# Kernel tuning notes

Hardware: AMD Instinct MI355X
Metric: run time of the kernel (lower is better)

Reference implementation:

```python
import jax, jax.numpy as jnp
import numpy as np
import math

MAX2D = 1001        # max_2d_position_embeddings
COORD = 128         # coordinate_size
SHAPE = 128         # shape_size
PE = 384            # pos_embed_size
HID = 768           # layout_hidden_size
PAD = 0             # pad_token_id
EPS = 1e-12
INIT = 1024         # sinusoidal init_size
BIG = 100000000


def sinusoidal_table(num_embeddings=INIT, dim=PE, padding_idx=PAD):
    half = dim // 2
    freq = np.exp(np.arange(half, dtype=np.float32) * (-math.log(10000.0) / (half - 1)))
    ang = np.arange(num_embeddings, dtype=np.float32)[:, None] * freq[None, :]
    tab = np.concatenate([np.sin(ang), np.cos(ang)], axis=1)
    if padding_idx is not None:
        tab[padding_idx, :] = 0.0
    return jnp.asarray(tab, dtype=jnp.float32)


def setup_inputs() -> dict:
    key = jax.random.key(0)
    ks = jax.random.split(key, 16)
    B, L = 2, 1024
    x1 = jax.random.randint(ks[0], (B, L), 0, 501, dtype=jnp.int32)
    y1 = jax.random.randint(ks[1], (B, L), 0, 501, dtype=jnp.int32)
    w = jax.random.randint(ks[2], (B, L), 0, 500, dtype=jnp.int32)
    h = jax.random.randint(ks[3], (B, L), 0, 500, dtype=jnp.int32)
    bbox = jnp.stack([x1, y1, x1 + w, y1 + h], axis=-1)  # [B,L,4], 0..1000
    attention_mask = jnp.ones((B, L), dtype=jnp.int32)
    s = 0.02
    inp = {
        'bbox': bbox,
        'attention_mask': attention_mask,
        'x_tab': jax.random.normal(ks[4], (MAX2D, COORD), jnp.float32) * s,
        'y_tab': jax.random.normal(ks[5], (MAX2D, COORD), jnp.float32) * s,
        'h_tab': jax.random.normal(ks[6], (MAX2D, SHAPE), jnp.float32) * s,
        'w_tab': jax.random.normal(ks[7], (MAX2D, SHAPE), jnp.float32) * s,
        'W_tl_w': jax.random.normal(ks[8], (HID, 2 * PE), jnp.float32) * s,
        'W_tl_b': jnp.zeros((HID,), jnp.float32),
        'W_tr_w': jax.random.normal(ks[9], (HID, 2 * PE), jnp.float32) * s,
        'W_tr_b': jnp.zeros((HID,), jnp.float32),
        'W_bl_w': jax.random.normal(ks[10], (HID, 2 * PE), jnp.float32) * s,
        'W_bl_b': jnp.zeros((HID,), jnp.float32),
        'W_br_w': jax.random.normal(ks[11], (HID, 2 * PE), jnp.float32) * s,
        'W_br_b': jnp.zeros((HID,), jnp.float32),
        'ln_g': jnp.ones((HID,), jnp.float32),
        'ln_b': jnp.zeros((HID,), jnp.float32),
        'params': 50,
    }
    return inp


def _knn_graph(bbox, mask, topk):
    # mask out padded boxes with a huge coordinate (matches masked_fill)
    bm = jnp.where((mask == 0)[..., None], BIG, bbox).astype(jnp.float32)
    xc = (bm[:, :, 0] + bm[:, :, 2]) / 2.0
    yc = (bm[:, :, 1] + bm[:, :, 3]) / 2.0
    dist = (xc[:, :, None] - xc[:, None, :]) ** 2 + (yc[:, :, None] - yc[:, None, :]) ** 2
    _, topk_index = jax.lax.top_k(-dist, topk)  # smallest distances
    topk_index = topk_index.astype(jnp.int32)
    B, L, _ = topk_index.shape
    lm = jnp.zeros((B, L, L), jnp.int32)
    b_ix = jnp.arange(B)[:, None, None]
    l_ix = jnp.arange(L)[None, :, None]
    lm = lm.at[b_ix, l_ix, topk_index].set(1)
    return topk_index, lm


def _rel_pos_emb(bbox, topk_index, sin_tab):
    # diff[b,i,k] = coord[b,i] - coord[b,topk_index[b,i,k]]
    gather = jax.vmap(lambda v, idx: v[idx])  # per-batch gather

    def diffs(c):
        d = c[:, :, None] - gather(c, topk_index)
        d = jnp.clip(d, 1 - MAX2D, MAX2D - 1)
        # torch negative indexing into the table wraps: idx % INIT
        return sin_tab[jnp.mod(d, INIT)]  # [B,L,K,PE]

    ex1 = diffs(bbox[:, :, 0])
    ey1 = diffs(bbox[:, :, 1])
    ex2 = diffs(bbox[:, :, 2])
    ey2 = diffs(bbox[:, :, 3])
    return ex1, ey1, ex2, ey2


def _linear(x, w, b):
    return jnp.einsum('blki,oi->blko', x, w) + b


def reference(bbox, attention_mask, x_tab, y_tab, h_tab, w_tab,
              W_tl_w, W_tl_b, W_tr_w, W_tr_b, W_bl_w, W_bl_b, W_br_w, W_br_b,
              ln_g, ln_b, params):
    sin_tab = sinusoidal_table()
    # spatial position embeddings
    layout_emb = jnp.concatenate([
        x_tab[bbox[:, :, 0]], y_tab[bbox[:, :, 1]],
        x_tab[bbox[:, :, 2]], y_tab[bbox[:, :, 3]],
        h_tab[bbox[:, :, 3] - bbox[:, :, 1]],
        w_tab[bbox[:, :, 2] - bbox[:, :, 0]],
    ], axis=-1)  # [B,L,HID]

    topk = min(bbox.shape[1], int(params))
    topk_index, local_mask = _knn_graph(bbox, attention_mask, topk)

    ex1, ey1, ex2, ey2 = _rel_pos_emb(bbox, topk_index, sin_tab)
    p = (_linear(jnp.concatenate([ex1, ey1], -1), W_tl_w, W_tl_b)
         + _linear(jnp.concatenate([ex2, ey1], -1), W_tr_w, W_tr_b)
         + _linear(jnp.concatenate([ex1, ey2], -1), W_bl_w, W_bl_b)
         + _linear(jnp.concatenate([ex2, ey2], -1), W_br_w, W_br_b))

    mu = jnp.mean(layout_emb, axis=-1, keepdims=True)
    var = jnp.mean((layout_emb - mu) ** 2, axis=-1, keepdims=True)
    layout_emb = (layout_emb - mu) / jnp.sqrt(var + EPS) * ln_g + ln_b
    # dropout is identity in eval mode
    return layout_emb, p, topk_index, local_mask
```

## Files before the change

### kernel.cpp

```cpp
#include <hip/hip_runtime.h>
#include <math.h>

namespace {
constexpr int B_ = 2;
constexpr int L_ = 1024;
constexpr int K_ = 50;
constexpr int HID_ = 768;
constexpr int PE_ = 384;
constexpr int HALF_ = 192;
constexpr int TROWS_ = 1024;

typedef float f32x4 __attribute__((ext_vector_type(4)));

constexpr long long OUT0 = 0;
constexpr long long OUT1 = OUT0 + (long long)B_ * L_ * HID_;
constexpr long long OUT2 = OUT1 + (long long)B_ * L_ * K_ * HID_;
constexpr long long OUT3 = OUT2 + (long long)B_ * L_ * K_;

constexpr long long WS_SIN = 0;
constexpr long long WS_T   = WS_SIN + (long long)TROWS_ * PE_;
constexpr long long WS_TI  = WS_T + 4LL * TROWS_ * HID_;
}

__global__ __launch_bounds__(192) void k_sin_tab(float* __restrict__ tab) {
    const int r = blockIdx.x;
    const int j = threadIdx.x;
    const float c = -0.04822168780092243f;
    float fr = expf((float)j * c);
    float ang = (float)r * fr;
    float s, co;
    if (r == 0) { s = 0.f; co = 0.f; } else { s = sinf(ang); co = cosf(ang); }
    tab[r * PE_ + j] = s;
    tab[r * PE_ + HALF_ + j] = co;
}

__global__ __launch_bounds__(256) void k_build_T(
    const float* __restrict__ sinT,
    const float* __restrict__ Wtl, const float* __restrict__ Wtr,
    const float* __restrict__ Wbl, const float* __restrict__ Wbr,
    const float* __restrict__ btl, const float* __restrict__ btr,
    const float* __restrict__ bbl, const float* __restrict__ bbr,
    float* __restrict__ Tout)
{
    const int t = blockIdx.z;
    const float* Wa; const float* Wb; int coff;
    if (t == 0)      { Wa = Wtl; Wb = Wbl; coff = 0; }
    else if (t == 1) { Wa = Wtr; Wb = Wbr; coff = 0; }
    else if (t == 2) { Wa = Wtl; Wb = Wtr; coff = PE_; }
    else             { Wa = Wbl; Wb = Wbr; coff = PE_; }

    __shared__ float As[32][65];
    __shared__ float Bs[32][65];
    const int tid = threadIdx.x;
    const int r0 = blockIdx.x * 64;
    const int o0 = blockIdx.y * 64;
    const int ty = tid >> 4, tx = tid & 15;
    float acc[4][4] = {{0.f, 0.f, 0.f, 0.f}, {0.f, 0.f, 0.f, 0.f},
                       {0.f, 0.f, 0.f, 0.f}, {0.f, 0.f, 0.f, 0.f}};

    for (int k0 = 0; k0 < PE_; k0 += 32) {
        #pragma unroll
        for (int s = 0; s < 8; ++s) {
            int l = s * 256 + tid;
            int rr = l >> 5, jj = l & 31;
            As[jj][rr] = sinT[(r0 + rr) * PE_ + k0 + jj];
            Bs[jj][rr] = Wa[(o0 + rr) * (2 * PE_) + coff + k0 + jj]
                       + Wb[(o0 + rr) * (2 * PE_) + coff + k0 + jj];
        }
        __syncthreads();
        #pragma unroll
        for (int kk = 0; kk < 32; ++kk) {
            float a[4], b[4];
            #pragma unroll
            for (int m = 0; m < 4; ++m) a[m] = As[kk][ty * 4 + m];
            #pragma unroll
            for (int n = 0; n < 4; ++n) b[n] = Bs[kk][tx * 4 + n];
            #pragma unroll
            for (int m = 0; m < 4; ++m)
                #pragma unroll
                for (int n = 0; n < 4; ++n)
                    acc[m][n] = fmaf(a[m], b[n], acc[m][n]);
        }
        __syncthreads();
    }

    #pragma unroll
    for (int m = 0; m < 4; ++m) {
        int r = r0 + ty * 4 + m;
        #pragma unroll
        for (int n = 0; n < 4; ++n) {
            int o = o0 + tx * 4 + n;
            float v = acc[m][n];
            if (t == 0) v += btl[o] + btr[o] + bbl[o] + bbr[o];
            Tout[(long long)t * TROWS_ * HID_ + (long long)r * HID_ + o] = v;
        }
    }
}

__device__ __forceinline__ float block_sum_256(float x, float* red) {
    #pragma unroll
    for (int off = 32; off > 0; off >>= 1) x += __shfl_xor(x, off, 64);
    const int wave = threadIdx.x >> 6;
    if ((threadIdx.x & 63) == 0) red[wave] = x;
    __syncthreads();
    float t = red[0] + red[1] + red[2] + red[3];
    __syncthreads();
    return t;
}

__global__ __launch_bounds__(256) void k_layout_emb(
    const int4* __restrict__ bbox, const float* __restrict__ xt,
    const float* __restrict__ yt, const float* __restrict__ ht,
    const float* __restrict__ wt, const float* __restrict__ g,
    const float* __restrict__ bb, float* __restrict__ out)
{
    __shared__ float red[4];
    const int tok = blockIdx.x;
    const int4 q = bbox[tok];
    const int tid = threadIdx.x;
    float v[3];
    #pragma unroll
    for (int s = 0; s < 3; ++s) {
        int e = tid + s * 256;
        int off = e & 127;
        int seg = e >> 7;
        float val;
        if (seg == 0)      val = xt[q.x * 128 + off];
        else if (seg == 1) val = yt[q.y * 128 + off];
        else if (seg == 2) val = xt[q.z * 128 + off];
        else if (seg == 3) val = yt[q.w * 128 + off];
        else if (seg == 4) val = ht[(q.w - q.y) * 128 + off];
        else               val = wt[(q.z - q.x) * 128 + off];
        v[s] = val;
    }
    float mu = block_sum_256(v[0] + v[1] + v[2], red) * (1.0f / 768.0f);
    float sq = 0.f;
    #pragma unroll
    for (int s = 0; s < 3; ++s) { float d = v[s] - mu; sq = fmaf(d, d, sq); }
    float var = block_sum_256(sq, red) * (1.0f / 768.0f);
    float inv = 1.0f / sqrtf(var + 1e-12f);
    float* orow = out + (long long)tok * HID_;
    #pragma unroll
    for (int s = 0; s < 3; ++s) {
        int e = tid + s * 256;
        __builtin_nontemporal_store((v[s] - mu) * inv * g[e] + bb[e], orow + e);
    }
}

__global__ __launch_bounds__(256) void k_topk(
    const int4* __restrict__ bbox, const int* __restrict__ am,
    float* __restrict__ topk_f, int* __restrict__ topk_i,
    float* __restrict__ mask)
{
    __shared__ float xs[L_], ys[L_];
    __shared__ float mrow_s[L_];
    __shared__ unsigned long long wmin[4];
    const int bx = blockIdx.x;
    const int b = bx >> 10;
    const int i = bx & 1023;
    const int tid = threadIdx.x;
    for (int j = tid; j < L_; j += 256) {
        int4 q = bbox[b * L_ + j];
        float x1, y1, x2, y2;
        if (am[b * L_ + j] == 0) { x1 = y1 = x2 = y2 = 1e8f; }
        else { x1 = (float)q.x; y1 = (float)q.y; x2 = (float)q.z; y2 = (float)q.w; }
        xs[j] = (x1 + x2) * 0.5f;
        ys[j] = (y1 + y2) * 0.5f;
        mrow_s[j] = 0.f;
    }
    __syncthreads();
    const float xq = xs[i], yq = ys[i];
    unsigned long long key[4];
    #pragma unroll
    for (int s = 0; s < 4; ++s) {
        int j = tid + s * 256;
        float dx = xq - xs[j], dy = yq - ys[j];
        float d = dx * dx + dy * dy;
        key[s] = ((unsigned long long)__float_as_uint(d) << 32) | (unsigned int)j;
    }
    const int lane = tid & 63, wave = tid >> 6;
    const long long obase = (long long)(b * L_ + i) * K_;
    for (int r = 0; r < K_; ++r) {
        unsigned long long m = key[0] < key[1] ? key[0] : key[1];
        unsigned long long m2 = key[2] < key[3] ? key[2] : key[3];
        if (m2 < m) m = m2;
        #pragma unroll
        for (int off = 1; off < 64; off <<= 1) {
            unsigned long long o = __shfl_xor(m, off, 64);
            if (o < m) m = o;
        }
        if (lane == 0) wmin[wave] = m;
        __syncthreads();
        unsigned long long mm = wmin[0] < wmin[1] ? wmin[0] : wmin[1];
        unsigned long long mb = wmin[2] < wmin[3] ? wmin[2] : wmin[3];
        if (mb < mm) mm = mb;
        if (tid == 0) {
            int w = (int)(mm & 0xffffffffu);
            topk_f[obase + r] = (float)w;
            topk_i[obase + r] = w;
            mrow_s[w] = 1.0f;
        }
        #pragma unroll
        for (int s = 0; s < 4; ++s) if (key[s] == mm) key[s] = ~0ULL;
        __syncthreads();
    }
    f32x4* mrow = (f32x4*)(mask + (long long)(b * L_ + i) * L_);
    const f32x4* src = (const f32x4*)mrow_s;
    __builtin_nontemporal_store(src[tid], mrow + tid);
}

__device__ __forceinline__ int wrapc(int d) {
    d = d < -1000 ? -1000 : (d > 1000 ? 1000 : d);
    return (d + 1024) & 1023;
}

__global__ __launch_bounds__(256) void k_passemble(
    const int4* __restrict__ bbox, const int* __restrict__ topk_i,
    const f32x4* __restrict__ T, float* __restrict__ p)
{
    const int row = blockIdx.x * 4 + (threadIdx.x >> 6);
    const int lane = threadIdx.x & 63;
    const int b = row / (L_ * K_);
    const int rem = row - b * (L_ * K_);
    const int i = rem / K_;
    const int j = topk_i[row];
    const int4 bi = bbox[b * L_ + i];
    const int4 bj = bbox[b * L_ + j];
    const f32x4* T1 = T + (long long)wrapc(bi.x - bj.x) * 192;
    const f32x4* T2 = T + 196608 + (long long)wrapc(bi.z - bj.z) * 192;
    const f32x4* T3 = T + 2 * 196608 + (long long)wrapc(bi.y - bj.y) * 192;
    const f32x4* T4 = T + 3 * 196608 + (long long)wrapc(bi.w - bj.w) * 192;
    f32x4* prow = (f32x4*)p + (long long)row * 192;
    #pragma unroll
    for (int u = 0; u < 3; ++u) {
        int f = lane + u * 64;
        f32x4 o = T1[f] + T2[f] + T3[f] + T4[f];
        __builtin_nontemporal_store(o, prow + f);
    }
}

extern "C" void kernel_launch(void* const* d_in, const int* in_sizes, int n_in,
                              void* d_out, int out_size, void* d_ws, size_t ws_size,
                              hipStream_t stream)
{
    const int4* bbox = (const int4*)d_in[0];
    const int* am    = (const int*)d_in[1];
    const float* xt  = (const float*)d_in[2];
    const float* yt  = (const float*)d_in[3];
    const float* ht  = (const float*)d_in[4];
    const float* wt  = (const float*)d_in[5];
    const float* Wtl = (const float*)d_in[6];
    const float* btl = (const float*)d_in[7];
    const float* Wtr = (const float*)d_in[8];
    const float* btr = (const float*)d_in[9];
    const float* Wbl = (const float*)d_in[10];
    const float* bbl = (const float*)d_in[11];
    const float* Wbr = (const float*)d_in[12];
    const float* bbr = (const float*)d_in[13];
    const float* lng = (const float*)d_in[14];
    const float* lnb = (const float*)d_in[15];

    float* out = (float*)d_out;
    float* ws = (float*)d_ws;
    float* sinT = ws + WS_SIN;
    float* T = ws + WS_T;
    int* topk_i = (int*)(ws + WS_TI);

    k_sin_tab<<<dim3(TROWS_), dim3(HALF_), 0, stream>>>(sinT);
    k_build_T<<<dim3(16, 12, 4), dim3(256), 0, stream>>>(
        sinT, Wtl, Wtr, Wbl, Wbr, btl, btr, bbl, bbr, T);
    k_layout_emb<<<dim3(B_ * L_), dim3(256), 0, stream>>>(
        bbox, xt, yt, ht, wt, lng, lnb, out + OUT0);
    k_topk<<<dim3(B_ * L_), dim3(256), 0, stream>>>(
        bbox, am, out + OUT2, topk_i, out + OUT3);
    k_passemble<<<dim3(B_ * L_ * K_ / 4), dim3(256), 0, stream>>>(
        bbox, topk_i, (const f32x4*)T, out + OUT1);
}
```

Before: 522.2 us.

## Merge table GEMM, top-k and layernorm kernels into one launch

```diff
diff --git a/kernel.cpp b/kernel.cpp
--- a/kernel.cpp
+++ b/kernel.cpp
@@ -20,6 +20,10 @@
 constexpr long long WS_SIN = 0;
 constexpr long long WS_T   = WS_SIN + (long long)TROWS_ * PE_;
 constexpr long long WS_TI  = WS_T + 4LL * TROWS_ * HID_;
+
+constexpr int GEMM_BLOCKS = 16 * 12 * 4;
+constexpr int TOPK_BLOCKS = B_ * L_;
+constexpr int LN_BLOCKS   = B_ * L_;
 }
 
 __global__ __launch_bounds__(192) void k_sin_tab(float* __restrict__ tab) {
@@ -34,68 +38,12 @@
     tab[r * PE_ + HALF_ + j] = co;
 }
 
-__global__ __launch_bounds__(256) void k_build_T(
-    const float* __restrict__ sinT,
-    const float* __restrict__ Wtl, const float* __restrict__ Wtr,
-    const float* __restrict__ Wbl, const float* __restrict__ Wbr,
-    const float* __restrict__ btl, const float* __restrict__ btr,
-    const float* __restrict__ bbl, const float* __restrict__ bbr,
-    float* __restrict__ Tout)
-{
-    const int t = blockIdx.z;
-    const float* Wa; const float* Wb; int coff;
-    if (t == 0)      { Wa = Wtl; Wb = Wbl; coff = 0; }
-    else if (t == 1) { Wa = Wtr; Wb = Wbr; coff = 0; }
-    else if (t == 2) { Wa = Wtl; Wb = Wtr; coff = PE_; }
-    else             { Wa = Wbl; Wb = Wbr; coff = PE_; }
-
-    __shared__ float As[32][65];
-    __shared__ float Bs[32][65];
-    const int tid = threadIdx.x;
-    const int r0 = blockIdx.x * 64;
-    const int o0 = blockIdx.y * 64;
-    const int ty = tid >> 4, tx = tid & 15;
-    float acc[4][4] = {{0.f, 0.f, 0.f, 0.f}, {0.f, 0.f, 0.f, 0.f},
-                       {0.f, 0.f, 0.f, 0.f}, {0.f, 0.f, 0.f, 0.f}};
-
-    for (int k0 = 0; k0 < PE_; k0 += 32) {
-        #pragma unroll
-        for (int s = 0; s < 8; ++s) {
-            int l = s * 256 + tid;
-            int rr = l >> 5, jj = l & 31;
-            As[jj][rr] = sinT[(r0 + rr) * PE_ + k0 + jj];
-            Bs[jj][rr] = Wa[(o0 + rr) * (2 * PE_) + coff + k0 + jj]
-                       + Wb[(o0 + rr) * (2 * PE_) + coff + k0 + jj];
-        }
-        __syncthreads();
-        #pragma unroll
-        for (int kk = 0; kk < 32; ++kk) {
-            float a[4], b[4];
-            #pragma unroll
-            for (int m = 0; m < 4; ++m) a[m] = As[kk][ty * 4 + m];
-            #pragma unroll
-            for (int n = 0; n < 4; ++n) b[n] = Bs[kk][tx * 4 + n];
-            #pragma unroll
-            for (int m = 0; m < 4; ++m)
-                #pragma unroll
-                for (int n = 0; n < 4; ++n)
-                    acc[m][n] = fmaf(a[m], b[n], acc[m][n]);
-        }
-        __syncthreads();
-    }
-
-    #pragma unroll
-    for (int m = 0; m < 4; ++m) {
-        int r = r0 + ty * 4 + m;
-        #pragma unroll
-        for (int n = 0; n < 4; ++n) {
-            int o = o0 + tx * 4 + n;
-            float v = acc[m][n];
-            if (t == 0) v += btl[o] + btr[o] + bbl[o] + bbr[o];
-            Tout[(long long)t * TROWS_ * HID_ + (long long)r * HID_ + o] = v;
-        }
-    }
-}
+union SMem {
+    struct { float As[32][68]; float Bs[32][68]; } g;
+    struct { float xs[L_]; float ys[L_]; float mrow[L_];
+             unsigned long long wmin[4]; } t;
+    struct { float red[4]; } l;
+};
 
 __device__ __forceinline__ float block_sum_256(float x, float* red) {
     #pragma unroll
@@ -108,105 +56,172 @@
     return t;
 }
 
-__global__ __launch_bounds__(256) void k_layout_emb(
-    const int4* __restrict__ bbox, const float* __restrict__ xt,
-    const float* __restrict__ yt, const float* __restrict__ ht,
-    const float* __restrict__ wt, const float* __restrict__ g,
-    const float* __restrict__ bb, float* __restrict__ out)
+__global__ __launch_bounds__(256) void k_mega(
+    const float* __restrict__ sinT,
+    const float* __restrict__ Wtl, const float* __restrict__ Wtr,
+    const float* __restrict__ Wbl, const float* __restrict__ Wbr,
+    const float* __restrict__ btl, const float* __restrict__ btr,
+    const float* __restrict__ bbl, const float* __restrict__ bbr,
+    float* __restrict__ Tout,
+    const int4* __restrict__ bbox, const int* __restrict__ am,
+    float* __restrict__ topk_f, int* __restrict__ topk_i, float* __restrict__ mask,
+    const float* __restrict__ xt, const float* __restrict__ yt,
+    const float* __restrict__ ht, const float* __restrict__ wt,
+    const float* __restrict__ lng, const float* __restrict__ lnb,
+    float* __restrict__ lout)
 {
-    __shared__ float red[4];
-    const int tok = blockIdx.x;
-    const int4 q = bbox[tok];
+    __shared__ SMem sm;
+    const int bid = blockIdx.x;
     const int tid = threadIdx.x;
-    float v[3];
-    #pragma unroll
-    for (int s = 0; s < 3; ++s) {
-        int e = tid + s * 256;
-        int off = e & 127;
-        int seg = e >> 7;
-        float val;
-        if (seg == 0)      val = xt[q.x * 128 + off];
-        else if (seg == 1) val = yt[q.y * 128 + off];
-        else if (seg == 2) val = xt[q.z * 128 + off];
-        else if (seg == 3) val = yt[q.w * 128 + off];
-        else if (seg == 4) val = ht[(q.w - q.y) * 128 + off];
-        else               val = wt[(q.z - q.x) * 128 + off];
-        v[s] = val;
-    }
-    float mu = block_sum_256(v[0] + v[1] + v[2], red) * (1.0f / 768.0f);
-    float sq = 0.f;
-    #pragma unroll
-    for (int s = 0; s < 3; ++s) { float d = v[s] - mu; sq = fmaf(d, d, sq); }
-    float var = block_sum_256(sq, red) * (1.0f / 768.0f);
-    float inv = 1.0f / sqrtf(var + 1e-12f);
-    float* orow = out + (long long)tok * HID_;
-    #pragma unroll
-    for (int s = 0; s < 3; ++s) {
-        int e = tid + s * 256;
-        __builtin_nontemporal_store((v[s] - mu) * inv * g[e] + bb[e], orow + e);
-    }
-}
-
-__global__ __launch_bounds__(256) void k_topk(
-    const int4* __restrict__ bbox, const int* __restrict__ am,
-    float* __restrict__ topk_f, int* __restrict__ topk_i,
-    float* __restrict__ mask)
-{
-    __shared__ float xs[L_], ys[L_];
-    __shared__ float mrow_s[L_];
-    __shared__ unsigned long long wmin[4];
-    const int bx = blockIdx.x;
-    const int b = bx >> 10;
-    const int i = bx & 1023;
-    const int tid = threadIdx.x;
-    for (int j = tid; j < L_; j += 256) {
-        int4 q = bbox[b * L_ + j];
-        float x1, y1, x2, y2;
-        if (am[b * L_ + j] == 0) { x1 = y1 = x2 = y2 = 1e8f; }
-        else { x1 = (float)q.x; y1 = (float)q.y; x2 = (float)q.z; y2 = (float)q.w; }
-        xs[j] = (x1 + x2) * 0.5f;
-        ys[j] = (y1 + y2) * 0.5f;
-        mrow_s[j] = 0.f;
-    }
-    __syncthreads();
-    const float xq = xs[i], yq = ys[i];
-    unsigned long long key[4];
-    #pragma unroll
-    for (int s = 0; s < 4; ++s) {
-        int j = tid + s * 256;
-        float dx = xq - xs[j], dy = yq - ys[j];
-        float d = dx * dx + dy * dy;
-        key[s] = ((unsigned long long)__float_as_uint(d) << 32) | (unsigned int)j;
-    }
-    const int lane = tid & 63, wave = tid >> 6;
-    const long long obase = (long long)(b * L_ + i) * K_;
-    for (int r = 0; r < K_; ++r) {
-        unsigned long long m = key[0] < key[1] ? key[0] : key[1];
-        unsigned long long m2 = key[2] < key[3] ? key[2] : key[3];
-        if (m2 < m) m = m2;
-        #pragma unroll
-        for (int off = 1; off < 64; off <<= 1) {
-            unsigned long long o = __shfl_xor(m, off, 64);
-            if (o < m) m = o;
-        }
-        if (lane == 0) wmin[wave] = m;
+
+    if (bid < GEMM_BLOCKS) {
+        const int t   = bid / 192;
+        const int rem = bid - t * 192;
+        const int rx  = rem & 15;
+        const int oy  = rem >> 4;
+        const float* Wa; const float* Wb; int coff;
+        if (t == 0)      { Wa = Wtl; Wb = Wbl; coff = 0; }
+        else if (t == 1) { Wa = Wtr; Wb = Wbr; coff = 0; }
+        else if (t == 2) { Wa = Wtl; Wb = Wtr; coff = PE_; }
+        else             { Wa = Wbl; Wb = Wbr; coff = PE_; }
+
+        const int r0 = rx * 64;
+        const int o0 = oy * 64;
+        const int ty = tid >> 4, tx = tid & 15;
+        float acc[4][4] = {{0.f,0.f,0.f,0.f},{0.f,0.f,0.f,0.f},
+                           {0.f,0.f,0.f,0.f},{0.f,0.f,0.f,0.f}};
+
+        for (int k0 = 0; k0 < PE_; k0 += 32) {
+            #pragma unroll
+            for (int s = 0; s < 2; ++s) {
+                int idx = s * 256 + tid;
+                int rr = idx >> 3, q = idx & 7;
+                f32x4 av = *(const f32x4*)&sinT[(r0 + rr) * PE_ + k0 + q * 4];
+                f32x4 w1 = *(const f32x4*)&Wa[(o0 + rr) * (2 * PE_) + coff + k0 + q * 4];
+                f32x4 w2 = *(const f32x4*)&Wb[(o0 + rr) * (2 * PE_) + coff + k0 + q * 4];
+                f32x4 bv = w1 + w2;
+                #pragma unroll
+                for (int c = 0; c < 4; ++c) {
+                    sm.g.As[q * 4 + c][rr] = av[c];
+                    sm.g.Bs[q * 4 + c][rr] = bv[c];
+                }
+            }
+            __syncthreads();
+            #pragma unroll
+            for (int kk = 0; kk < 32; ++kk) {
+                f32x4 a = *(const f32x4*)&sm.g.As[kk][ty * 4];
+                f32x4 b = *(const f32x4*)&sm.g.Bs[kk][tx * 4];
+                #pragma unroll
+                for (int m = 0; m < 4; ++m)
+                    #pragma unroll
+                    for (int n = 0; n < 4; ++n)
+                        acc[m][n] = fmaf(a[m], b[n], acc[m][n]);
+            }
+            __syncthreads();
+        }
+
+        #pragma unroll
+        for (int m = 0; m < 4; ++m) {
+            int r = r0 + ty * 4 + m;
+            f32x4 v;
+            #pragma unroll
+            for (int n = 0; n < 4; ++n) {
+                int o = o0 + tx * 4 + n;
+                float x = acc[m][n];
+                if (t == 0) x += btl[o] + btr[o] + bbl[o] + bbr[o];
+                v[n] = x;
+            }
+            *(f32x4*)&Tout[(long long)t * TROWS_ * HID_ + (long long)r * HID_ + o0 + tx * 4] = v;
+        }
+        return;
+    }
+
+    if (bid < GEMM_BLOCKS + TOPK_BLOCKS) {
+        const int bi = bid - GEMM_BLOCKS;
+        const int b = bi >> 10;
+        const int i = bi & 1023;
+        for (int j = tid; j < L_; j += 256) {
+            int4 q = bbox[b * L_ + j];
+            float x1, y1, x2, y2;
+            if (am[b * L_ + j] == 0) { x1 = y1 = x2 = y2 = 1e8f; }
+            else { x1 = (float)q.x; y1 = (float)q.y; x2 = (float)q.z; y2 = (float)q.w; }
+            sm.t.xs[j] = (x1 + x2) * 0.5f;
+            sm.t.ys[j] = (y1 + y2) * 0.5f;
+            sm.t.mrow[j] = 0.f;
+        }
         __syncthreads();
-        unsigned long long mm = wmin[0] < wmin[1] ? wmin[0] : wmin[1];
-        unsigned long long mb = wmin[2] < wmin[3] ? wmin[2] : wmin[3];
-        if (mb < mm) mm = mb;
-        if (tid == 0) {
-            int w = (int)(mm & 0xffffffffu);
-            topk_f[obase + r] = (float)w;
-            topk_i[obase + r] = w;
-            mrow_s[w] = 1.0f;
-        }
-        #pragma unroll
-        for (int s = 0; s < 4; ++s) if (key[s] == mm) key[s] = ~0ULL;
-        __syncthreads();
-    }
-    f32x4* mrow = (f32x4*)(mask + (long long)(b * L_ + i) * L_);
-    const f32x4* src = (const f32x4*)mrow_s;
-    __builtin_nontemporal_store(src[tid], mrow + tid);
+        const float xq = sm.t.xs[i], yq = sm.t.ys[i];
+        unsigned long long key[4];
+        #pragma unroll
+        for (int s = 0; s < 4; ++s) {
+            int j = tid + s * 256;
+            float dx = xq - sm.t.xs[j], dy = yq - sm.t.ys[j];
+            float d = dx * dx + dy * dy;
+            key[s] = ((unsigned long long)__float_as_uint(d) << 32) | (unsigned int)j;
+        }
+        const int lane = tid & 63, wave = tid >> 6;
+        const long long obase = (long long)(b * L_ + i) * K_;
+        for (int r = 0; r < K_; ++r) {
+            unsigned long long m = key[0] < key[1] ? key[0] : key[1];
+            unsigned long long m2 = key[2] < key[3] ? key[2] : key[3];
+            if (m2 < m) m = m2;
+            #pragma unroll
+            for (int off = 1; off < 64; off <<= 1) {
+                unsigned long long o = __shfl_xor(m, off, 64);
+                if (o < m) m = o;
+            }
+            if (lane == 0) sm.t.wmin[wave] = m;
+            __syncthreads();
+            unsigned long long mm = sm.t.wmin[0] < sm.t.wmin[1] ? sm.t.wmin[0] : sm.t.wmin[1];
+            unsigned long long mb = sm.t.wmin[2] < sm.t.wmin[3] ? sm.t.wmin[2] : sm.t.wmin[3];
+            if (mb < mm) mm = mb;
+            if (tid == 0) {
+                int w = (int)(mm & 0xffffffffu);
+                topk_f[obase + r] = (float)w;
+                topk_i[obase + r] = w;
+                sm.t.mrow[w] = 1.0f;
+            }
+            #pragma unroll
+            for (int s = 0; s < 4; ++s) if (key[s] == mm) key[s] = ~0ULL;
+            __syncthreads();
+        }
+        f32x4* mrow = (f32x4*)(mask + (long long)(b * L_ + i) * L_);
+        const f32x4* src = (const f32x4*)sm.t.mrow;
+        __builtin_nontemporal_store(src[tid], mrow + tid);
+        return;
+    }
+
+    {
+        const int tok = bid - (GEMM_BLOCKS + TOPK_BLOCKS);
+        const int4 q = bbox[tok];
+        float v[3];
+        #pragma unroll
+        for (int s = 0; s < 3; ++s) {
+            int e = tid + s * 256;
+            int off = e & 127;
+            int seg = e >> 7;
+            float val;
+            if (seg == 0)      val = xt[q.x * 128 + off];
+            else if (seg == 1) val = yt[q.y * 128 + off];
+            else if (seg == 2) val = xt[q.z * 128 + off];
+            else if (seg == 3) val = yt[q.w * 128 + off];
+            else if (seg == 4) val = ht[(q.w - q.y) * 128 + off];
+            else               val = wt[(q.z - q.x) * 128 + off];
+            v[s] = val;
+        }
+        float mu = block_sum_256(v[0] + v[1] + v[2], sm.l.red) * (1.0f / 768.0f);
+        float sq = 0.f;
+        #pragma unroll
+        for (int s = 0; s < 3; ++s) { float d = v[s] - mu; sq = fmaf(d, d, sq); }
+        float var = block_sum_256(sq, sm.l.red) * (1.0f / 768.0f);
+        float inv = 1.0f / sqrtf(var + 1e-12f);
+        float* orow = lout + (long long)tok * HID_;
+        #pragma unroll
+        for (int s = 0; s < 3; ++s) {
+            int e = tid + s * 256;
+            __builtin_nontemporal_store((v[s] - mu) * inv * lng[e] + lnb[e], orow + e);
+        }
+    }
 }
 
 __device__ __forceinline__ int wrapc(int d) {
@@ -267,12 +282,10 @@
     int* topk_i = (int*)(ws + WS_TI);
 
     k_sin_tab<<<dim3(TROWS_), dim3(HALF_), 0, stream>>>(sinT);
-    k_build_T<<<dim3(16, 12, 4), dim3(256), 0, stream>>>(
-        sinT, Wtl, Wtr, Wbl, Wbr, btl, btr, bbl, bbr, T);
-    k_layout_emb<<<dim3(B_ * L_), dim3(256), 0, stream>>>(
-        bbox, xt, yt, ht, wt, lng, lnb, out + OUT0);
-    k_topk<<<dim3(B_ * L_), dim3(256), 0, stream>>>(
-        bbox, am, out + OUT2, topk_i, out + OUT3);
+    k_mega<<<dim3(GEMM_BLOCKS + TOPK_BLOCKS + LN_BLOCKS), dim3(256), 0, stream>>>(
+        sinT, Wtl, Wtr, Wbl, Wbr, btl, btr, bbl, bbr, T,
+        bbox, am, out + OUT2, topk_i, out + OUT3,
+        xt, yt, ht, wt, lng, lnb, out + OUT0);
     k_passemble<<<dim3(B_ * L_ * K_ / 4), dim3(256), 0, stream>>>(
         bbox, topk_i, (const f32x4*)T, out + OUT1);
 }
```

Result: no change. 528.4 us (+1.2%).
